# Kernel optimization log

Measured on AMD Instinct MI355X. Metric: run time of the kernel, lower is better.

## Reference

```python
import jax, jax.numpy as jnp
import numpy as np

B, N, DIM = 8, 2048, 1024
EPSILON = 0.03
SCALE = 1.0 / np.sqrt(DIM).astype(np.float32)


def setup_inputs() -> dict:
    key = jax.random.key(0)
    ks = jax.random.split(key, 5)
    Q = jax.random.normal(ks[0], (B, N, DIM), dtype=jnp.float32)
    K = jax.random.normal(ks[1], (B, N, DIM), dtype=jnp.float32)
    V = jax.random.normal(ks[2], (B, N, DIM), dtype=jnp.float32)
    # H_net: Linear(dim, dim//2) -> SiLU -> Linear(dim//2, 1); init like torch default scale-ish
    W1 = jax.random.normal(ks[3], (DIM, DIM // 2), dtype=jnp.float32) * (1.0 / np.sqrt(DIM))
    b1 = jnp.zeros((DIM // 2,), dtype=jnp.float32)
    W2 = jax.random.normal(ks[4], (DIM // 2, 1), dtype=jnp.float32) * (1.0 / np.sqrt(DIM // 2))
    b2 = jnp.zeros((1,), dtype=jnp.float32)
    return {"Q": Q, "K": K, "V": V, "W1": W1, "b1": b1, "W2": W2, "b2": b2}


def _mlp(x, W1, b1, W2, b2):
    h = jax.nn.silu(x @ W1 + b1)  # [B,N,dim//2]
    return h @ W2 + b2            # [B,N,1]


def reference(Q, K, V, W1, b1, W2, b2):
    def energy(q, v):
        # scores [B,N,N]
        A = jax.nn.softmax(jnp.einsum('bnd,bmd->bnm', q, K) * SCALE, axis=-1)
        attn_out = jnp.einsum('bnm,bmd->bnd', A, v)
        H = jnp.sum(_mlp(attn_out, W1, b1, W2, b2))
        return H, attn_out

    # grads of scalar energy H w.r.t. Q and V (dH_dV is computed per the
    # original code but discarded by the final split; only dH_dQ survives)
    (dH_dQ, dH_dV), attn_out = jax.grad(energy, argnums=(0, 1), has_aux=True)(Q, V)
    # S_new = cat([Q,V]) + eps*cat([dH_dV, -dH_dQ]); split -> V_new = V - eps*dH_dQ
    V_new = V - EPSILON * dH_dQ
    return V_new + attn_out
```

## Files before the change

kernel.cpp:

```cpp
#include <hip/hip_runtime.h>

typedef __bf16 bf16;
typedef __attribute__((ext_vector_type(8))) __bf16 bf16x8;
typedef __attribute__((ext_vector_type(4))) float f32x4;

#define MEMFENCE asm volatile("" ::: "memory")

__device__ __forceinline__ void gload16(const bf16* g, bf16* l) {
    __builtin_amdgcn_global_load_lds(
        (const __attribute__((address_space(1))) void*)g,
        (__attribute__((address_space(3))) void*)l,
        16, 0, 0);
}

template<int EPI>
__global__ __launch_bounds__(512, 1)
void gemm8p(const bf16* __restrict__ A, const bf16* __restrict__ Bm,
            void* __restrict__ Cp, int Kdim, int lda, int ldb, int ldc,
            long sA, long sB, long sC, float alpha,
            const float* __restrict__ aux1, const bf16* __restrict__ aux3)
{
    __shared__ __align__(16) char smem[131072];

    const int gx = gridDim.x, gy = gridDim.y;
    int lin = blockIdx.x + gx * (blockIdx.y + gy * blockIdx.z);
    const int q = (gx * gy * gridDim.z) >> 3;
    lin = (lin & 7) * q + (lin >> 3);
    const int bx = lin % gx;
    const int rem0 = lin / gx;
    const int by = rem0 % gy;
    const int bz = rem0 / gy;

    const int t0 = threadIdx.x;
    const int w = t0 >> 6, lane = t0 & 63;
    const int wm = w >> 2, wn = w & 3;
    const int m0 = by * 256, n0 = bx * 256;
    const long zb = bz;

    const bf16* Ab = A  + zb * sA + (size_t)m0 * lda;
    const bf16* Bb = Bm + zb * sB + (size_t)n0 * ldb;

    const int sr16 = lane >> 2;
    const int sce  = ((((lane & 3) << 4) ^ (((lane >> 5) & 1) << 5))) >> 1;
    const int r0s = (w >> 1) * 16 + sr16;
    const int c0s = (w & 1) * 32 + sce;
    const bf16* gA0 = Ab + (size_t)r0s * lda + c0s;
    const bf16* gA1 = Ab + (size_t)(128 + r0s) * lda + c0s;
    const bf16* gB0 = Bb + (size_t)r0s * ldb + c0s;
    const bf16* gB1 = Bb + (size_t)(128 + r0s) * ldb + c0s;
    const size_t a64 = (size_t)64 * lda, b64 = (size_t)64 * ldb;
    const int ldsW0 = w * 1024, ldsW1 = (8 + w) * 1024;

    const int lr = lane & 15, lkq = lane >> 4;
    const int phx = ((lane >> 3) & 1) << 5;
    const int frag_base = (lr * 64 + lkq * 16) ^ phx;
    const char* aR = smem + wm * 16384 + frag_base;
    const char* bR = smem + 32768 + (wn >> 1) * 16384 + (wn & 1) * 8192 + frag_base;

    f32x4 acc[8][4] = {};
    const int NTt = Kdim >> 6;

    auto stgA = [&](int h, int u, int p) {
        char* L = smem + p * 65536 + h * 16384;
        const bf16* g = h ? gA1 : gA0;
        gload16(g + (size_t)u * 64,        (bf16*)(L + ldsW0));
        gload16(g + a64 + (size_t)u * 64,  (bf16*)(L + ldsW1));
    };
    auto stgB = [&](int h, int u, int p) {
        char* L = smem + p * 65536 + 32768 + h * 16384;
        const bf16* g = h ? gB1 : gB0;
        gload16(g + (size_t)u * 64,        (bf16*)(L + ldsW0));
        gload16(g + b64 + (size_t)u * 64,  (bf16*)(L + ldsW1));
    };

    stgA(0, 0, 0); stgA(1, 0, 0); stgB(0, 0, 0); stgB(1, 0, 0);
    stgB(0, 1, 1); stgB(1, 1, 1);
    asm volatile("s_waitcnt vmcnt(4)" ::: "memory");
    __builtin_amdgcn_s_barrier();
    MEMFENCE;

    bf16x8 a[4][2], b[4][2];

#define QUAD(MFB, NFB)                                                                  \
    __builtin_amdgcn_s_setprio(1);                                                      \
    _Pragma("unroll")                                                                   \
    for (int ks = 0; ks < 2; ++ks)                                                      \
        _Pragma("unroll")                                                               \
        for (int mf = 0; mf < 4; ++mf)                                                  \
            _Pragma("unroll")                                                           \
            for (int nf = 0; nf < 2; ++nf)                                              \
                acc[(MFB) + mf][(NFB) + nf] = __builtin_amdgcn_mfma_f32_16x16x32_bf16(  \
                    a[mf][ks], b[(NFB) + nf][ks], acc[(MFB) + mf][(NFB) + nf], 0, 0, 0);\
    __builtin_amdgcn_s_setprio(0);

    for (int u = 0; u < NTt; ++u) {
        const int p = u & 1;
        const char* aP = aR + p * 65536;
        const char* bP = bR + p * 65536;
        const bool st1 = (u + 1 < NTt), st2 = (u + 2 < NTt);

        if (st1) stgA(0, u + 1, p ^ 1);
        #pragma unroll
        for (int mf = 0; mf < 4; ++mf)
            #pragma unroll
            for (int ks = 0; ks < 2; ++ks)
                a[mf][ks] = *(const bf16x8*)(aP + (mf * 2 + ks) * 1024);
        #pragma unroll
        for (int nf = 0; nf < 2; ++nf)
            #pragma unroll
            for (int ks = 0; ks < 2; ++ks)
                b[nf][ks] = *(const bf16x8*)(bP + (nf * 2 + ks) * 1024);
        MEMFENCE;
        __builtin_amdgcn_s_barrier();
        QUAD(0, 0)
        MEMFENCE;
        __builtin_amdgcn_s_barrier();

        if (st1) stgA(1, u + 1, p ^ 1);
        #pragma unroll
        for (int nf = 2; nf < 4; ++nf)
            #pragma unroll
            for (int ks = 0; ks < 2; ++ks)
                b[nf][ks] = *(const bf16x8*)(bP + (nf * 2 + ks) * 1024);
        MEMFENCE;
        __builtin_amdgcn_s_barrier();
        QUAD(0, 2)
        MEMFENCE;
        __builtin_amdgcn_s_barrier();

        if (st2) stgB(0, u + 2, p);
        #pragma unroll
        for (int mf = 0; mf < 4; ++mf)
            #pragma unroll
            for (int ks = 0; ks < 2; ++ks)
                a[mf][ks] = *(const bf16x8*)(aP + ((4 + mf) * 2 + ks) * 1024);
        MEMFENCE;
        __builtin_amdgcn_s_barrier();
        QUAD(4, 2)
        MEMFENCE;
        __builtin_amdgcn_s_barrier();

        if (st2) stgB(1, u + 2, p);
        MEMFENCE;
        if (st2) asm volatile("s_waitcnt vmcnt(4)" ::: "memory");
        else     asm volatile("s_waitcnt vmcnt(0)" ::: "memory");
        __builtin_amdgcn_s_barrier();
        QUAD(4, 0)
        MEMFENCE;
        __builtin_amdgcn_s_barrier();
        MEMFENCE;
    }
#undef QUAD

    const int rb  = m0 + wm * 128 + lkq * 4;
    const int cb0 = n0 + wn * 64 + lr;
    #pragma unroll
    for (int mf = 0; mf < 8; ++mf) {
        #pragma unroll
        for (int r = 0; r < 4; ++r) {
            const int rw = rb + mf * 16 + r;
            float rd = 0.f;
            if (EPI == 1) rd = aux1[zb * 2048 + rw];
            #pragma unroll
            for (int nf = 0; nf < 4; ++nf) {
                const int c = cb0 + nf * 16;
                const size_t ix = (size_t)rw * ldc + c;
                const float v = acc[mf][nf][r];
                if (EPI == 0) {
                    ((bf16*)Cp + zb * sC)[ix] = (bf16)(alpha * v);
                } else if (EPI == 1) {
                    bf16* Cb = (bf16*)Cp + zb * sC;
                    const bf16* Am = aux3 + zb * sC;
                    Cb[ix] = (bf16)((float)Am[ix] * (v - rd));
                } else {
                    float* C = (float*)Cp + zb * sC;
                    const float* Vv = aux1 + zb * sC;
                    const bf16* AOv = aux3 + zb * sC;
                    C[ix] = Vv[ix] + (float)AOv[ix] - alpha * v;
                }
            }
        }
    }
}

template<int EPI, int NF>
__global__ __launch_bounds__(512, 1)
void gemm_nc(const bf16* __restrict__ A, const bf16* __restrict__ Bm,
             void* __restrict__ Cp, int Kdim, int lda, int ldb, int ldc,
             long sA, long sB, long sC, float alpha,
             const float* __restrict__ aux1, const float* __restrict__ aux2,
             const bf16* __restrict__ aux3)
{
    constexpr int SB = NF * 4096;
    __shared__ __align__(16) char smem[65536 + 4 * SB];

    const int gx = gridDim.x, gy = gridDim.y;
    int lin = blockIdx.x + gx * (blockIdx.y + gy * blockIdx.z);
    const int q = (gx * gy * gridDim.z) >> 3;
    lin = (lin & 7) * q + (lin >> 3);
    const int bx = lin % gx;
    const int rem0 = lin / gx;
    const int by = rem0 % gy;
    const int bz = rem0 / gy;

    const int t0 = threadIdx.x;
    const int w = t0 >> 6, lane = t0 & 63;
    const int wm = w >> 2, wn = w & 3;
    const int m0 = by * 256, n0 = bx * (64 * NF);
    const long zb = bz;

    const bf16* Ab = A  + zb * sA + (size_t)m0 * lda;
    const bf16* Bb = Bm + zb * sB + (size_t)n0 * ldb;

    const int sr16 = lane >> 2;
    const int sce  = ((((lane & 3) << 4) ^ (((lane >> 5) & 1) << 5))) >> 1;
    const int stg0 = w * 2, stg1 = w * 2 + 1;
    const bf16* pA0 = Ab + (size_t)(stg0 * 16 + sr16) * lda + sce;
    const bf16* pA1 = Ab + (size_t)(stg1 * 16 + sr16) * lda + sce;
    const bf16* pB0 = Bb + (size_t)((NF == 4 ? stg0 : w) * 16 + sr16) * ldb + sce;
    const bf16* pB1 = Bb + (size_t)(stg1 * 16 + sr16) * ldb + sce;

    const int lr = lane & 15, lkq = lane >> 4;
    const int phx = ((lane >> 3) & 1) << 5;
    const int frag_base = lr * 64 + lkq * 16;

    f32x4 acc[8][NF] = {};
    const int NT = Kdim >> 5;

    auto issueSlot = [&](int p) {
        char* lA = smem + (p & 3) * 16384;
        char* lB = smem + 65536 + (p & 3) * SB;
        const int kt = p << 5;
        gload16(pA0 + kt, (bf16*)(lA + stg0 * 1024));
        gload16(pA1 + kt, (bf16*)(lA + stg1 * 1024));
        if (NF == 4) {
            gload16(pB0 + kt, (bf16*)(lB + stg0 * 1024));
            gload16(pB1 + kt, (bf16*)(lB + stg1 * 1024));
        } else {
            gload16(pB0 + kt, (bf16*)(lB + w * 1024));
        }
    };
    auto rdA = [&](const char* base, int sub) {
        return *(const bf16x8*)(base + (((sub << 10) + frag_base) ^ phx));
    };

    issueSlot(0); issueSlot(1); issueSlot(2);
    if (NF == 4) asm volatile("s_waitcnt vmcnt(4)" ::: "memory");
    else         asm volatile("s_waitcnt vmcnt(3)" ::: "memory");
    __builtin_amdgcn_s_barrier();
    MEMFENCE;

    bf16x8 alo[4], ahi[4], b0[NF], b1[NF];
    {
        const char* cA = smem;
        const char* cB = smem + 65536;
        #pragma unroll
        for (int mf = 0; mf < 4; ++mf) alo[mf] = rdA(cA, wm * 8 + mf);
        #pragma unroll
        for (int nf = 0; nf < NF; ++nf) b0[nf] = rdA(cB, wn * NF + nf);
    }

    auto stepBody = [&](int SL, int s, bf16x8 (&bA)[NF], bf16x8 (&bB)[NF]) {
        if (s + 3 < NT) issueSlot(s + 3);
        const char* cA = smem + SL * 16384;
        #pragma unroll
        for (int mf = 0; mf < 4; ++mf) ahi[mf] = rdA(cA, wm * 8 + 4 + mf);

        __builtin_amdgcn_s_setprio(1);
        #pragma unroll
        for (int mf = 0; mf < 4; ++mf)
            #pragma unroll
            for (int nf = 0; nf < NF; ++nf)
                acc[mf][nf] = __builtin_amdgcn_mfma_f32_16x16x32_bf16(alo[mf], bA[nf], acc[mf][nf], 0, 0, 0);
        __builtin_amdgcn_s_setprio(0);

        if (s + 1 < NT) {
            const int NS = (SL + 1) & 3;
            const char* nA = smem + NS * 16384;
            const char* nB = smem + 65536 + NS * SB;
            #pragma unroll
            for (int mf = 0; mf < 4; ++mf) alo[mf] = rdA(nA, wm * 8 + mf);
            #pragma unroll
            for (int nf = 0; nf < NF; ++nf) bB[nf] = rdA(nB, wn * NF + nf);
        }

        __builtin_amdgcn_s_setprio(1);
        #pragma unroll
        for (int mf = 0; mf < 4; ++mf)
            #pragma unroll
            for (int nf = 0; nf < NF; ++nf)
                acc[4 + mf][nf] = __builtin_amdgcn_mfma_f32_16x16x32_bf16(ahi[mf], bA[nf], acc[4 + mf][nf], 0, 0, 0);
        __builtin_amdgcn_s_setprio(0);

        MEMFENCE;
        if (s + 3 < NT) {
            if (NF == 4) asm volatile("s_waitcnt vmcnt(4)" ::: "memory");
            else         asm volatile("s_waitcnt vmcnt(3)" ::: "memory");
        } else {
            asm volatile("s_waitcnt vmcnt(0)" ::: "memory");
        }
        __builtin_amdgcn_s_barrier();
        MEMFENCE;
    };

    for (int s = 0; s < NT; s += 2) {
        stepBody(s & 3, s, b0, b1);
        stepBody((s + 1) & 3, s + 1, b1, b0);
    }

    const int rb  = m0 + wm * 128 + lkq * 4;
    const int cb0 = n0 + wn * (NF * 16) + lr;
    #pragma unroll
    for (int mf = 0; mf < 8; ++mf) {
        #pragma unroll
        for (int nf = 0; nf < NF; ++nf) {
            const int c = cb0 + nf * 16;
            #pragma unroll
            for (int r = 0; r < 4; ++r) {
                const int rw = rb + mf * 16 + r;
                const size_t ix = (size_t)rw * ldc + c;
                const float v = acc[mf][nf][r];
                if (EPI == 0) {
                    ((bf16*)Cp + zb * sC)[ix] = (bf16)(alpha * v);
                } else {
                    const float u = v + aux1[c];
                    const float sg = 1.f / (1.f + __expf(-u));
                    const float dd = sg * (1.f + u * (1.f - sg));
                    ((bf16*)Cp)[ix] = (bf16)(dd * aux2[c]);
                    ((bf16*)aux3)[ix] = (bf16)v;
                }
            }
        }
    }
}

template<bool DN, bool DT>
__global__ __launch_bounds__(256)
void transcast_k(const float* __restrict__ in, bf16* __restrict__ outN,
                 bf16* __restrict__ outT, int R, int C)
{
    __shared__ float ts[64][65];
    const int t = threadIdx.x;
    const int c0 = blockIdx.x * 64, r0 = blockIdx.y * 64;
    const size_t zoff = (size_t)blockIdx.z * R * C;

    const int rr = t >> 2, cc = (t & 3) * 16;
    float4 f[4];
    const float* src = in + zoff + (size_t)(r0 + rr) * C + c0 + cc;
    #pragma unroll
    for (int i = 0; i < 4; ++i) f[i] = *(const float4*)(src + 4 * i);

    if (DN) {
        bf16x8 h0, h1;
        #pragma unroll
        for (int i = 0; i < 2; ++i) {
            h0[i*4+0] = (bf16)f[i].x;   h0[i*4+1] = (bf16)f[i].y;
            h0[i*4+2] = (bf16)f[i].z;   h0[i*4+3] = (bf16)f[i].w;
            h1[i*4+0] = (bf16)f[i+2].x; h1[i*4+1] = (bf16)f[i+2].y;
            h1[i*4+2] = (bf16)f[i+2].z; h1[i*4+3] = (bf16)f[i+2].w;
        }
        bf16* dst = outN + zoff + (size_t)(r0 + rr) * C + c0 + cc;
        *(bf16x8*)dst = h0;
        *(bf16x8*)(dst + 8) = h1;
    }
    if (DT) {
        #pragma unroll
        for (int i = 0; i < 4; ++i) {
            ts[rr][cc + 4*i + 0] = f[i].x;
            ts[rr][cc + 4*i + 1] = f[i].y;
            ts[rr][cc + 4*i + 2] = f[i].z;
            ts[rr][cc + 4*i + 3] = f[i].w;
        }
        __syncthreads();
        const int ct = t >> 2, rr4 = (t & 3) * 16;
        bf16x8 o0, o1;
        #pragma unroll
        for (int i = 0; i < 8; ++i) o0[i] = (bf16)ts[rr4 + i][ct];
        #pragma unroll
        for (int i = 0; i < 8; ++i) o1[i] = (bf16)ts[rr4 + 8 + i][ct];
        bf16* dst = outT + zoff + (size_t)(c0 + ct) * R + r0 + rr4;
        *(bf16x8*)dst = o0;
        *(bf16x8*)(dst + 8) = o1;
    }
}

__global__ __launch_bounds__(256)
void softmax_k(const bf16* __restrict__ S, bf16* __restrict__ A)
{
    const size_t row = blockIdx.x;
    const int t = threadIdx.x;
    const int wid = t >> 6, lane = t & 63;
    __shared__ float r1[4], r2[4];

    bf16x8 v = *(const bf16x8*)(S + row * 2048 + t * 8);
    float f[8];
    float mx = -1e30f;
    #pragma unroll
    for (int i = 0; i < 8; ++i) { f[i] = (float)v[i]; mx = fmaxf(mx, f[i]); }
    #pragma unroll
    for (int o = 32; o; o >>= 1) mx = fmaxf(mx, __shfl_xor(mx, o, 64));
    if (!lane) r1[wid] = mx;
    __syncthreads();
    mx = fmaxf(fmaxf(r1[0], r1[1]), fmaxf(r1[2], r1[3]));

    float sum = 0.f;
    #pragma unroll
    for (int i = 0; i < 8; ++i) { f[i] = __expf(f[i] - mx); sum += f[i]; }
    #pragma unroll
    for (int o = 32; o; o >>= 1) sum += __shfl_xor(sum, o, 64);
    if (!lane) r2[wid] = sum;
    __syncthreads();
    sum = r2[0] + r2[1] + r2[2] + r2[3];

    const float inv = 1.f / sum;
    bf16x8 ov;
    #pragma unroll
    for (int i = 0; i < 8; ++i) ov[i] = (bf16)(f[i] * inv);
    *(bf16x8*)(A + row * 2048 + t * 8) = ov;
}

__global__ __launch_bounds__(256)
void rowdot_k(const bf16* __restrict__ U, const bf16* __restrict__ H, float* __restrict__ rd)
{
    const int r = blockIdx.x * 4 + (threadIdx.x >> 6);
    const int lane = threadIdx.x & 63;
    bf16x8 uv = *(const bf16x8*)(U + (size_t)r * 512 + lane * 8);
    bf16x8 hv = *(const bf16x8*)(H + (size_t)r * 512 + lane * 8);
    float d = 0.f;
    #pragma unroll
    for (int i = 0; i < 8; ++i) d += (float)uv[i] * (float)hv[i];
    #pragma unroll
    for (int o = 32; o; o >>= 1) d += __shfl_xor(d, o, 64);
    if (!lane) rd[r] = d;
}

extern "C" void kernel_launch(void* const* d_in, const int* in_sizes, int n_in,
                              void* d_out, int out_size, void* d_ws, size_t ws_size,
                              hipStream_t stream)
{
    const float* Q  = (const float*)d_in[0];
    const float* Km = (const float*)d_in[1];
    const float* V  = (const float*)d_in[2];
    const float* W1 = (const float*)d_in[3];
    const float* b1 = (const float*)d_in[4];
    const float* W2 = (const float*)d_in[5];
    float* out = (float*)d_out;

    char* ws = (char*)d_ws;
    bf16* Amat = (bf16*)(ws);
    bf16* AO   = (bf16*)(ws + 67108864);
    bf16* Kb   = AO;
    bf16* KbT  = (bf16*)(ws + 100663296);
    bf16* Vb   = (bf16*)(ws + 134217728);
    bf16* Hb   = Vb;
    bf16* VbT  = (bf16*)(ws + 167772160);
    bf16* U    = VbT;
    bf16* Qb   = (bf16*)(ws + 201326592);
    bf16* VW1b = Qb;
    bf16* W1T  = (bf16*)(ws + 234881024);
    float* rowdot = (float*)(ws + 235929600);
    bf16* S    = (bf16*)d_out;

    const long sQK = 2048L * 1024;
    const long sS  = 2048L * 2048;
    const long sVW = 2048L * 512;
    dim3 blk(256), blkG(512);

    transcast_k<true,  false><<<dim3(16, 32, 8), blk, 0, stream>>>(Q,  Qb, nullptr, 2048, 1024);
    transcast_k<true,  true ><<<dim3(16, 32, 8), blk, 0, stream>>>(Km, Kb, KbT,     2048, 1024);
    transcast_k<true,  true ><<<dim3(16, 32, 8), blk, 0, stream>>>(V,  Vb, VbT,     2048, 1024);
    transcast_k<false, true ><<<dim3(8,  16, 1), blk, 0, stream>>>(W1, nullptr, W1T, 1024, 512);

    gemm8p<0><<<dim3(8, 8, 8), blkG, 0, stream>>>(
        Qb, Kb, S, 1024, 1024, 1024, 2048, sQK, sQK, sS, 0.03125f, nullptr, nullptr);

    gemm_nc<0, 2><<<dim3(4, 8, 8), blkG, 0, stream>>>(
        Vb, W1T, VW1b, 1024, 1024, 1024, 512, sQK, 0, sVW, 1.0f, nullptr, nullptr, nullptr);

    softmax_k<<<dim3(16384), blk, 0, stream>>>(S, Amat);

    gemm8p<0><<<dim3(4, 8, 8), blkG, 0, stream>>>(
        Amat, VbT, AO, 2048, 2048, 2048, 1024, sS, sQK, sQK, 1.0f, nullptr, nullptr);

    gemm_nc<3, 2><<<dim3(4, 64, 1), blkG, 0, stream>>>(
        AO, W1T, U, 1024, 1024, 1024, 512, 0, 0, 0, 1.0f, b1, W2, Hb);

    rowdot_k<<<dim3(4096), blk, 0, stream>>>(U, Hb, rowdot);

    gemm8p<1><<<dim3(8, 8, 8), blkG, 0, stream>>>(
        U, VW1b, Amat, 512, 512, 512, 2048, sVW, sVW, sS, 1.0f, rowdot, Amat);

    gemm8p<2><<<dim3(4, 8, 8), blkG, 0, stream>>>(
        Amat, KbT, out, 2048, 2048, 2048, 1024, sS, sQK, sQK, 0.03f * 0.03125f, V, AO);
}
```

Before: 430.4 us.

## Replace 256x256 eight-wave GEMM with 128x128 four-wave multi-block GEMM

Swaps the large 256x256-tile, 512-thread, 128KB-LDS GEMM (fine-grained barrier-interleaved pipeline, K-step 64) for a simpler 128x128 tile, 256-thread kernel with 32KB LDS and K-step 32, allowing up to three blocks per CU. The aim is more resident blocks for latency hiding and better wave balance across CUs in place of a hand-tuned single-block schedule. In exchange, per-block data reuse drops, global/LDS traffic per FLOP doubles, and each K-step now waits on vmcnt(0) with a full barrier.

```diff
diff --git a/kernel.cpp b/kernel.cpp
--- a/kernel.cpp
+++ b/kernel.cpp
@@ -14,13 +14,13 @@
 }
 
 template<int EPI>
-__global__ __launch_bounds__(512, 1)
-void gemm8p(const bf16* __restrict__ A, const bf16* __restrict__ Bm,
+__global__ __launch_bounds__(256, 3)
+void gemm2b(const bf16* __restrict__ A, const bf16* __restrict__ Bm,
             void* __restrict__ Cp, int Kdim, int lda, int ldb, int ldc,
             long sA, long sB, long sC, float alpha,
             const float* __restrict__ aux1, const bf16* __restrict__ aux3)
 {
-    __shared__ __align__(16) char smem[131072];
+    __shared__ __align__(16) char smem[32768];
 
     const int gx = gridDim.x, gy = gridDim.y;
     int lin = blockIdx.x + gx * (blockIdx.y + gy * blockIdx.z);
@@ -33,8 +33,8 @@
 
     const int t0 = threadIdx.x;
     const int w = t0 >> 6, lane = t0 & 63;
-    const int wm = w >> 2, wn = w & 3;
-    const int m0 = by * 256, n0 = bx * 256;
+    const int wm = w >> 1, wn = w & 1;
+    const int m0 = by * 128, n0 = bx * 128;
     const long zb = bz;
 
     const bf16* Ab = A  + zb * sA + (size_t)m0 * lda;
@@ -42,120 +42,60 @@
 
     const int sr16 = lane >> 2;
     const int sce  = ((((lane & 3) << 4) ^ (((lane >> 5) & 1) << 5))) >> 1;
-    const int r0s = (w >> 1) * 16 + sr16;
-    const int c0s = (w & 1) * 32 + sce;
-    const bf16* gA0 = Ab + (size_t)r0s * lda + c0s;
-    const bf16* gA1 = Ab + (size_t)(128 + r0s) * lda + c0s;
-    const bf16* gB0 = Bb + (size_t)r0s * ldb + c0s;
-    const bf16* gB1 = Bb + (size_t)(128 + r0s) * ldb + c0s;
-    const size_t a64 = (size_t)64 * lda, b64 = (size_t)64 * ldb;
-    const int ldsW0 = w * 1024, ldsW1 = (8 + w) * 1024;
+    const bf16* gA = Ab + (size_t)sr16 * lda + sce;
+    const bf16* gB = Bb + (size_t)sr16 * ldb + sce;
 
     const int lr = lane & 15, lkq = lane >> 4;
     const int phx = ((lane >> 3) & 1) << 5;
     const int frag_base = (lr * 64 + lkq * 16) ^ phx;
-    const char* aR = smem + wm * 16384 + frag_base;
-    const char* bR = smem + 32768 + (wn >> 1) * 16384 + (wn & 1) * 8192 + frag_base;
-
-    f32x4 acc[8][4] = {};
-    const int NTt = Kdim >> 6;
-
-    auto stgA = [&](int h, int u, int p) {
-        char* L = smem + p * 65536 + h * 16384;
-        const bf16* g = h ? gA1 : gA0;
-        gload16(g + (size_t)u * 64,        (bf16*)(L + ldsW0));
-        gload16(g + a64 + (size_t)u * 64,  (bf16*)(L + ldsW1));
+
+    f32x4 acc[4][4] = {};
+    const int NT = Kdim >> 5;
+
+    auto stage = [&](int u, int p) {
+        char* L = smem + p * 16384;
+        const size_t ku = (size_t)u * 32;
+        gload16(gA + (size_t)(w    ) * 16 * lda + ku, (bf16*)(L + w * 1024));
+        gload16(gA + (size_t)(w + 4) * 16 * lda + ku, (bf16*)(L + (w + 4) * 1024));
+        gload16(gB + (size_t)(w    ) * 16 * ldb + ku, (bf16*)(L + 8192 + w * 1024));
+        gload16(gB + (size_t)(w + 4) * 16 * ldb + ku, (bf16*)(L + 8192 + (w + 4) * 1024));
     };
-    auto stgB = [&](int h, int u, int p) {
-        char* L = smem + p * 65536 + 32768 + h * 16384;
-        const bf16* g = h ? gB1 : gB0;
-        gload16(g + (size_t)u * 64,        (bf16*)(L + ldsW0));
-        gload16(g + b64 + (size_t)u * 64,  (bf16*)(L + ldsW1));
-    };
-
-    stgA(0, 0, 0); stgA(1, 0, 0); stgB(0, 0, 0); stgB(1, 0, 0);
-    stgB(0, 1, 1); stgB(1, 1, 1);
-    asm volatile("s_waitcnt vmcnt(4)" ::: "memory");
+
+    stage(0, 0);
+    asm volatile("s_waitcnt vmcnt(0)" ::: "memory");
     __builtin_amdgcn_s_barrier();
     MEMFENCE;
 
-    bf16x8 a[4][2], b[4][2];
-
-#define QUAD(MFB, NFB)                                                                  \
-    __builtin_amdgcn_s_setprio(1);                                                      \
-    _Pragma("unroll")                                                                   \
-    for (int ks = 0; ks < 2; ++ks)                                                      \
-        _Pragma("unroll")                                                               \
-        for (int mf = 0; mf < 4; ++mf)                                                  \
-            _Pragma("unroll")                                                           \
-            for (int nf = 0; nf < 2; ++nf)                                              \
-                acc[(MFB) + mf][(NFB) + nf] = __builtin_amdgcn_mfma_f32_16x16x32_bf16(  \
-                    a[mf][ks], b[(NFB) + nf][ks], acc[(MFB) + mf][(NFB) + nf], 0, 0, 0);\
-    __builtin_amdgcn_s_setprio(0);
-
-    for (int u = 0; u < NTt; ++u) {
+    for (int u = 0; u < NT; ++u) {
         const int p = u & 1;
-        const char* aP = aR + p * 65536;
-        const char* bP = bR + p * 65536;
-        const bool st1 = (u + 1 < NTt), st2 = (u + 2 < NTt);
-
-        if (st1) stgA(0, u + 1, p ^ 1);
+        if (u + 1 < NT) stage(u + 1, p ^ 1);
+
+        const char* aBuf = smem + p * 16384 + frag_base;
+        const char* bBuf = aBuf + 8192;
+        bf16x8 a[4], b[4];
+        #pragma unroll
+        for (int mf = 0; mf < 4; ++mf) a[mf] = *(const bf16x8*)(aBuf + (wm * 4 + mf) * 1024);
+        #pragma unroll
+        for (int nf = 0; nf < 4; ++nf) b[nf] = *(const bf16x8*)(bBuf + (wn * 4 + nf) * 1024);
+
+        __builtin_amdgcn_s_setprio(1);
         #pragma unroll
         for (int mf = 0; mf < 4; ++mf)
             #pragma unroll
-            for (int ks = 0; ks < 2; ++ks)
-                a[mf][ks] = *(const bf16x8*)(aP + (mf * 2 + ks) * 1024);
-        #pragma unroll
-        for (int nf = 0; nf < 2; ++nf)
-            #pragma unroll
-            for (int ks = 0; ks < 2; ++ks)
-                b[nf][ks] = *(const bf16x8*)(bP + (nf * 2 + ks) * 1024);
+            for (int nf = 0; nf < 4; ++nf)
+                acc[mf][nf] = __builtin_amdgcn_mfma_f32_16x16x32_bf16(a[mf], b[nf], acc[mf][nf], 0, 0, 0);
+        __builtin_amdgcn_s_setprio(0);
+
         MEMFENCE;
-        __builtin_amdgcn_s_barrier();
-        QUAD(0, 0)
-        MEMFENCE;
-        __builtin_amdgcn_s_barrier();
-
-        if (st1) stgA(1, u + 1, p ^ 1);
-        #pragma unroll
-        for (int nf = 2; nf < 4; ++nf)
-            #pragma unroll
-            for (int ks = 0; ks < 2; ++ks)
-                b[nf][ks] = *(const bf16x8*)(bP + (nf * 2 + ks) * 1024);
-        MEMFENCE;
-        __builtin_amdgcn_s_barrier();
-        QUAD(0, 2)
-        MEMFENCE;
-        __builtin_amdgcn_s_barrier();
-
-        if (st2) stgB(0, u + 2, p);
-        #pragma unroll
-        for (int mf = 0; mf < 4; ++mf)
-            #pragma unroll
-            for (int ks = 0; ks < 2; ++ks)
-                a[mf][ks] = *(const bf16x8*)(aP + ((4 + mf) * 2 + ks) * 1024);
-        MEMFENCE;
-        __builtin_amdgcn_s_barrier();
-        QUAD(4, 2)
-        MEMFENCE;
-        __builtin_amdgcn_s_barrier();
-
-        if (st2) stgB(1, u + 2, p);
-        MEMFENCE;
-        if (st2) asm volatile("s_waitcnt vmcnt(4)" ::: "memory");
-        else     asm volatile("s_waitcnt vmcnt(0)" ::: "memory");
-        __builtin_amdgcn_s_barrier();
-        QUAD(4, 0)
-        MEMFENCE;
+        if (u + 1 < NT) asm volatile("s_waitcnt vmcnt(0)" ::: "memory");
         __builtin_amdgcn_s_barrier();
         MEMFENCE;
     }
-#undef QUAD
-
-    const int rb  = m0 + wm * 128 + lkq * 4;
+
+    const int rb  = m0 + wm * 64 + lkq * 4;
     const int cb0 = n0 + wn * 64 + lr;
     #pragma unroll
-    for (int mf = 0; mf < 8; ++mf) {
+    for (int mf = 0; mf < 4; ++mf) {
         #pragma unroll
         for (int r = 0; r < 4; ++r) {
             const int rw = rb + mf * 16 + r;
@@ -471,7 +411,7 @@
     transcast_k<true,  true ><<<dim3(16, 32, 8), blk, 0, stream>>>(V,  Vb, VbT,     2048, 1024);
     transcast_k<false, true ><<<dim3(8,  16, 1), blk, 0, stream>>>(W1, nullptr, W1T, 1024, 512);
 
-    gemm8p<0><<<dim3(8, 8, 8), blkG, 0, stream>>>(
+    gemm2b<0><<<dim3(16, 16, 8), blk, 0, stream>>>(
         Qb, Kb, S, 1024, 1024, 1024, 2048, sQK, sQK, sS, 0.03125f, nullptr, nullptr);
 
     gemm_nc<0, 2><<<dim3(4, 8, 8), blkG, 0, stream>>>(
@@ -479,7 +419,7 @@
 
     softmax_k<<<dim3(16384), blk, 0, stream>>>(S, Amat);
 
-    gemm8p<0><<<dim3(4, 8, 8), blkG, 0, stream>>>(
+    gemm2b<0><<<dim3(8, 16, 8), blk, 0, stream>>>(
         Amat, VbT, AO, 2048, 2048, 2048, 1024, sS, sQK, sQK, 1.0f, nullptr, nullptr);
 
     gemm_nc<3, 2><<<dim3(4, 64, 1), blkG, 0, stream>>>(
@@ -487,9 +427,9 @@
 
     rowdot_k<<<dim3(4096), blk, 0, stream>>>(U, Hb, rowdot);
 
-    gemm8p<1><<<dim3(8, 8, 8), blkG, 0, stream>>>(
+    gemm2b<1><<<dim3(16, 16, 8), blk, 0, stream>>>(
         U, VW1b, Amat, 512, 512, 512, 2048, sVW, sVW, sS, 1.0f, rowdot, Amat);
 
-    gemm8p<2><<<dim3(4, 8, 8), blkG, 0, stream>>>(
+    gemm2b<2><<<dim3(8, 16, 8), blk, 0, stream>>>(
         Amat, KbT, out, 2048, 2048, 2048, 1024, sS, sQK, sQK, 0.03f * 0.03125f, V, AO);
 }
```

Result: slower. 491.4 us (+14.2%).
